# Optimization experiments

Measured on AMD Instinct MI355X. Metric: run time of the kernel, lower is better.

## Reference

```python
import math
import jax, jax.numpy as jnp
import numpy as np

N_HEADS = 16
N_KV_HEADS = 4
HEAD_DIM = 128
D_MODEL = 2048
THETA = 10000.0
SCALE_BASE = 512


def _rope_cos_sin(seq_len, head_dim, theta):
    half = head_dim // 2
    inv_freq = 1.0 / theta ** (jnp.arange(half, dtype=jnp.float32) / half)
    pos = jnp.arange(seq_len, dtype=jnp.float32)
    freqs = jnp.outer(pos, inv_freq)  # (S, half)
    freqs = jnp.concatenate([freqs, freqs], axis=-1)  # (S, D)
    return jnp.cos(freqs), jnp.sin(freqs)


def _rotate_half(x):
    half = x.shape[-1] // 2
    return jnp.concatenate([-x[..., half:], x[..., :half]], axis=-1)


def _xpos_scale(seq_len, head_dim, scale_base):
    pos = jnp.arange(seq_len, dtype=jnp.float32)
    scale = (pos + scale_base / 2.0) / scale_base  # (S,)
    half = head_dim // 2
    s = jnp.broadcast_to(scale[:, None], (seq_len, half))
    # interleave: even idx -> scale, odd idx -> 1/scale
    return jnp.stack([s, 1.0 / s], axis=-1).reshape(seq_len, head_dim)


def setup_inputs() -> dict:
    key = jax.random.key(0)
    ks = jax.random.split(key, 5)
    std = 1.0 / math.sqrt(D_MODEL)
    x = jax.random.normal(ks[0], (2, 2048, D_MODEL), dtype=jnp.float32)
    Wq = jax.random.normal(ks[1], (D_MODEL, N_HEADS * HEAD_DIM), dtype=jnp.float32) * std
    Wk = jax.random.normal(ks[2], (D_MODEL, N_KV_HEADS * HEAD_DIM), dtype=jnp.float32) * std
    Wv = jax.random.normal(ks[3], (D_MODEL, N_KV_HEADS * HEAD_DIM), dtype=jnp.float32) * std
    Wo = jax.random.normal(ks[4], (N_HEADS * HEAD_DIM, D_MODEL), dtype=jnp.float32) * std
    return {"x": x, "Wq": Wq, "Wk": Wk, "Wv": Wv, "Wo": Wo}


def reference(x, Wq, Wk, Wv, Wo):
    B, S, _ = x.shape
    kv_groups = N_HEADS // N_KV_HEADS

    q = (x @ Wq).reshape(B, S, N_HEADS, HEAD_DIM).transpose(0, 2, 1, 3)     # (B,H,S,D)
    k = (x @ Wk).reshape(B, S, N_KV_HEADS, HEAD_DIM).transpose(0, 2, 1, 3)  # (B,Hk,S,D)
    v = (x @ Wv).reshape(B, S, N_KV_HEADS, HEAD_DIM).transpose(0, 2, 1, 3)

    cos, sin = _rope_cos_sin(S, HEAD_DIM, THETA)
    cos = cos[None, None]
    sin = sin[None, None]
    q = q * cos + _rotate_half(q) * sin
    k = k * cos + _rotate_half(k) * sin
    xscale = _xpos_scale(S, HEAD_DIM, SCALE_BASE)[None, None]
    q = q * xscale
    k = k * (1.0 / xscale)

    # GQA: expand kv heads to full head count
    k = jnp.repeat(k, kv_groups, axis=1)  # (B,H,S,D)
    v = jnp.repeat(v, kv_groups, axis=1)

    scale = math.sqrt(HEAD_DIM)
    scores = jnp.einsum('bhqd,bhkd->bhqk', q, k) / scale
    causal = jnp.tril(jnp.ones((S, S), dtype=bool))
    scores = jnp.where(causal[None, None], scores, -jnp.inf)
    attn = jax.nn.softmax(scores, axis=-1)
    out = jnp.einsum('bhqk,bhkd->bhqd', attn, v)
    out = out.transpose(0, 2, 1, 3).reshape(B, S, N_HEADS * HEAD_DIM)
    return out @ Wo
```

## Files before the change

kernel.cpp:

```cpp
#include <hip/hip_runtime.h>
#include <math.h>

#define BDIM 2
#define SLEN 2048
#define NH 16
#define NKV 4
#define HD 128

typedef __attribute__((ext_vector_type(8))) short short8v;
typedef __attribute__((ext_vector_type(4))) short short4v;
typedef __attribute__((ext_vector_type(8))) __bf16 bf16x8;
typedef __attribute__((ext_vector_type(4))) float f32x4;
typedef __attribute__((ext_vector_type(16))) float f32x16;
typedef __attribute__((ext_vector_type(4))) unsigned int u32x4;

__device__ inline unsigned short f2bf(float x) {
  unsigned int u = __builtin_bit_cast(unsigned int, x);
  unsigned int r = (u + 0x7fffu + ((u >> 16) & 1u)) >> 16;
  return (unsigned short)r;
}
__device__ inline float bf2f(unsigned short b) {
  unsigned int u = ((unsigned int)b) << 16;
  return __builtin_bit_cast(float, u);
}
__device__ inline unsigned int pk2(float a, float b) {
  unsigned short ua = __builtin_bit_cast(unsigned short, (__bf16)a);
  unsigned short ub = __builtin_bit_cast(unsigned short, (__bf16)b);
  return (unsigned int)ua | ((unsigned int)ub << 16);
}

template <bool BF16_OUT, bool SPLIT>
__global__ __launch_bounds__(256) void gemm_ring(
    const unsigned short* __restrict__ A, const unsigned short* __restrict__ Bt,
    void* __restrict__ C0, void* __restrict__ C1,
    int M, int N, int K, int Nsplit, int S0, int S1) {
  __shared__ __align__(16) unsigned short lds[3 * 8192];
  const int t    = threadIdx.x;
  const int lane = t & 63;
  const int w    = t >> 6;
  const int lg   = lane >> 4, l15 = lane & 15;
  const int wr   = w >> 1,    wc  = w & 1;
  const int bm = blockIdx.y * 128, bn = blockIdx.x * 128;

  const int r0  = t >> 2;
  const int c8  = (t & 3) ^ (r0 & 3);
  const int dst = t * 8;

#define STAGE(kt, b)                                                           \
  { _Pragma("unroll") for (int i = 0; i < 2; ++i) {                            \
      __builtin_amdgcn_global_load_lds(                                        \
          (const __attribute__((address_space(1))) unsigned int*)              \
              &A[(size_t)(bm + i * 64 + r0) * K + (kt) * 32 + c8 * 8],         \
          (__attribute__((address_space(3))) unsigned int*)                    \
              &lds[(b) * 8192 + i * 2048 + dst],                               \
          16, 0, 0);                                                           \
      __builtin_amdgcn_global_load_lds(                                        \
          (const __attribute__((address_space(1))) unsigned int*)              \
              &Bt[(size_t)(bn + i * 64 + r0) * K + (kt) * 32 + c8 * 8],        \
          (__attribute__((address_space(3))) unsigned int*)                    \
              &lds[(b) * 8192 + 4096 + i * 2048 + dst],                        \
          16, 0, 0);                                                           \
  } }

  f32x4 acc[4][4];
#pragma unroll
  for (int m = 0; m < 4; ++m)
#pragma unroll
    for (int n = 0; n < 4; ++n) acc[m][n] = (f32x4){0.f, 0.f, 0.f, 0.f};

  const int NT = K >> 5;
  STAGE(0, 0)
  STAGE(1, 1)
  int bc = 0;

  for (int kt = 0; kt < NT; ++kt) {
    if (kt + 1 < NT) {
      asm volatile("s_waitcnt vmcnt(4)" ::: "memory");
    } else {
      asm volatile("s_waitcnt vmcnt(0)" ::: "memory");
    }
    __builtin_amdgcn_s_barrier();
    __builtin_amdgcn_sched_barrier(0);

    const unsigned short* As = &lds[bc * 8192];
    const unsigned short* Bs = As + 4096;
    bf16x8 a[4], b[4];
#pragma unroll
    for (int m = 0; m < 4; ++m) {
      const int row = wr * 64 + m * 16 + l15;
      a[m] = __builtin_bit_cast(bf16x8, *reinterpret_cast<const short8v*>(
          &As[row * 32 + ((lg ^ (l15 & 3)) * 8)]));
    }
#pragma unroll
    for (int n = 0; n < 4; ++n) {
      const int row = wc * 64 + n * 16 + l15;
      b[n] = __builtin_bit_cast(bf16x8, *reinterpret_cast<const short8v*>(
          &Bs[row * 32 + ((lg ^ (l15 & 3)) * 8)]));
    }
#pragma unroll
    for (int m = 0; m < 4; ++m)
#pragma unroll
      for (int n = 0; n < 4; ++n)
        acc[m][n] = __builtin_amdgcn_mfma_f32_16x16x32_bf16(a[m], b[n], acc[m][n], 0, 0, 0);

    asm volatile("s_waitcnt lgkmcnt(0)" ::: "memory");
    __builtin_amdgcn_s_barrier();
    __builtin_amdgcn_sched_barrier(0);
    if (kt + 2 < NT) {
      const int nb = bc + 2 >= 3 ? bc - 1 : bc + 2;
      STAGE(kt + 2, nb)
    }
    bc = (bc + 1 >= 3) ? 0 : bc + 1;
  }

  void* dst_p;
  int col0, stride;
  if (!SPLIT || bn < Nsplit) {
    dst_p = C0; col0 = bn; stride = S0;
  } else {
    dst_p = C1; col0 = bn - Nsplit; stride = S1;
  }
#pragma unroll
  for (int m = 0; m < 4; ++m) {
#pragma unroll
    for (int j = 0; j < 4; ++j) {
      const size_t row = (size_t)(bm + wr * 64 + m * 16 + lg * 4 + j);
#pragma unroll
      for (int n = 0; n < 4; ++n) {
        const int col = col0 + wc * 64 + n * 16 + l15;
        if (BF16_OUT)
          ((unsigned short*)dst_p)[row * stride + col] = f2bf(acc[m][n][j]);
        else
          ((float*)dst_p)[row * stride + col] = acc[m][n][j];
      }
    }
  }
#undef STAGE
}

__global__ __launch_bounds__(256) void transpose_cast(
    const float* __restrict__ W, unsigned short* __restrict__ Wt, int K, int N) {
  __shared__ float tile[32][33];
  const int tx = threadIdx.x & 31, ty = threadIdx.x >> 5;
  const int n0 = blockIdx.x * 32, k0 = blockIdx.y * 32;
#pragma unroll
  for (int i = 0; i < 4; ++i)
    tile[ty + i * 8][tx] = W[(size_t)(k0 + ty + i * 8) * N + n0 + tx];
  __syncthreads();
#pragma unroll
  for (int i = 0; i < 4; ++i)
    Wt[(size_t)(n0 + ty + i * 8) * K + k0 + tx] = f2bf(tile[tx][ty + i * 8]);
}

__global__ __launch_bounds__(256) void cast_f32_bf16(
    const float* __restrict__ in, unsigned short* __restrict__ out) {
  const int i = (blockIdx.x * 256 + threadIdx.x) * 8;
  float4 a = *reinterpret_cast<const float4*>(&in[i]);
  float4 b = *reinterpret_cast<const float4*>(&in[i + 4]);
  short8v s;
  s[0] = f2bf(a.x); s[1] = f2bf(a.y); s[2] = f2bf(a.z); s[3] = f2bf(a.w);
  s[4] = f2bf(b.x); s[5] = f2bf(b.y); s[6] = f2bf(b.z); s[7] = f2bf(b.w);
  *reinterpret_cast<short8v*>(&out[i]) = s;
}

__global__ __launch_bounds__(256) void rope_xpos_ip(
    unsigned short* __restrict__ buf, int row_stride, int nh_shift, int invert,
    float extra_scale) {
  const int idx = blockIdx.x * 256 + threadIdx.x;
  const int dp  = idx & 63;
  const int tmp = idx >> 6;
  const int h   = tmp & ((1 << nh_shift) - 1);
  const int row = tmp >> nh_shift;
  const int s   = row & (SLEN - 1);

  const float inv_freq = expf(-(float)dp * (9.210340371976184f / 64.0f));
  const float ang = (float)s * inv_freq;
  float sn, cs;
  sincosf(ang, &sn, &cs);

  unsigned short* p = buf + (size_t)row * row_stride + h * HD;
  const float x0 = bf2f(p[dp]);
  const float x1 = bf2f(p[dp + 64]);
  float y0 = x0 * cs - x1 * sn;
  float y1 = x1 * cs + x0 * sn;

  const float scl = ((float)s + 256.0f) / 512.0f;
  float se_even = invert ? (1.0f / scl) : scl;
  float se_odd  = invert ? scl : (1.0f / scl);
  float se = ((dp & 1) ? se_odd : se_even) * extra_scale;

  p[dp]      = f2bf(y0 * se);
  p[dp + 64] = f2bf(y1 * se);
}

__global__ __launch_bounds__(512) void flash_attn_v10(
    const unsigned short* __restrict__ qb, const unsigned short* __restrict__ kvb,
    unsigned short* __restrict__ o) {
  const int bid = blockIdx.x;
  const int u   = bid & 7;
  const int bh  = bid >> 3;
  const int h   = bh & (NH - 1);
  const int b   = bh >> 4;
  const int kvh = h >> 2;

  __shared__ __align__(16) unsigned char smem[131072];

  const int t    = threadIdx.x;
  const int lane = t & 63;
  const int w    = t >> 6;
  const int par  = w >> 2;
  const int wq   = w & 3;
  const int hi   = lane >> 5;
  const int l31  = lane & 31;

  const size_t bS = (size_t)b * SLEN;

  const int vr2 = t & 31;
  const int vg  = t >> 5;
  int krow[2], kgrp[2];
#pragma unroll
  for (int i = 0; i < 2; ++i) {
    const int slot = w * 2048 + i * 1024 + lane * 16;
    krow[i] = slot >> 8;
    kgrp[i] = (slot >> 4) & 15;
  }

#define K_STAGE(kt, bufk)                                                      \
  { _Pragma("unroll") for (int i = 0; i < 2; ++i) {                            \
      const unsigned short* ksrc = &kvb[(bS + (size_t)(kt) * 64 + krow[i]) * 1024 \
          + kvh * 128 + ((kgrp[i] ^ (krow[i] & 15)) << 3)];                    \
      __builtin_amdgcn_global_load_lds(                                        \
          (const __attribute__((address_space(1))) unsigned int*)ksrc,         \
          (__attribute__((address_space(3))) unsigned int*)                    \
              (smem + (bufk) * 16384 + w * 2048 + i * 1024),                   \
          16, 0, 0); } }

#define V_LOAD(kt, r0, r1)                                                     \
  { const size_t vb_ = (bS + (size_t)(kt) * 64) * 1024 + kvh * 128 + 512;      \
    r0 = *reinterpret_cast<const short8v*>(                                    \
        &kvb[vb_ + (size_t)(2 * vr2) * 1024 + vg * 8]);                        \
    r1 = *reinterpret_cast<const short8v*>(                                    \
        &kvb[vb_ + (size_t)(2 * vr2 + 1) * 1024 + vg * 8]); }

#define V_WRITE(bufk, r0, r1)                                                  \
  { unsigned int* Vw_ = (unsigned int*)(smem + 65536 + (bufk) * 16384);        \
    _Pragma("unroll") for (int j = 0; j < 8; ++j) {                            \
      const int d = vg * 8 + j;                                                \
      Vw_[d * 32 + (vr2 ^ ((d & 7) << 2))] =                                   \
          (unsigned int)(unsigned short)r0[j] |                                \
          ((unsigned int)(unsigned short)r1[j] << 16); } }

  for (int half = 0; half < 2; ++half) {
    const int qt2 = half ? (15 - u) : u;

    bf16x8 qf[8];
    {
      const size_t qrow = (bS + qt2 * 128 + wq * 32 + l31) * 2048 + (size_t)h * HD;
#pragma unroll
      for (int c = 0; c < 8; ++c)
        qf[c] = __builtin_bit_cast(bf16x8,
            *reinterpret_cast<const short8v*>(&qb[qrow + c * 16 + hi * 8]));
    }

    f32x16 Od[4];
#pragma unroll
    for (int ds = 0; ds < 4; ++ds)
#pragma unroll
      for (int r = 0; r < 16; ++r) Od[ds][r] = 0.f;
    float m_run = -1e30f, l_run = 0.f;

    short8v va0, va1, vb0, vb1;

    K_STAGE(0, 0)
    K_STAGE(1, 1)
    V_LOAD(0, va0, va1)
    V_LOAD(1, vb0, vb1)
    V_WRITE(0, va0, va1)
    V_WRITE(1, vb0, vb1)
    __syncthreads();

    for (int e = 0; e <= qt2; ++e) {
      const int s = e & 1;
      const int kt = 2 * e + par;
      const bool more = (e < qt2);
      if (more) {
        K_STAGE(2 * e + 2, (s ^ 1) * 2 + 0)
        K_STAGE(2 * e + 3, (s ^ 1) * 2 + 1)
        V_LOAD(2 * e + 2, va0, va1)
        V_LOAD(2 * e + 3, vb0, vb1)
      }
      const unsigned short* Kb = (const unsigned short*)(smem + (s * 2 + par) * 16384);
      const unsigned int*   Vw = (const unsigned int*)(smem + 65536 + (s * 2 + par) * 16384);

      f32x16 Sa, Sb;
#pragma unroll
      for (int r = 0; r < 16; ++r) { Sa[r] = 0.f; Sb[r] = 0.f; }
      __builtin_amdgcn_s_setprio(1);
#pragma unroll
      for (int c = 0; c < 8; ++c) {
        const int ra = l31, rb = 32 + l31;
        bf16x8 ka = __builtin_bit_cast(bf16x8, *reinterpret_cast<const short8v*>(
            &Kb[ra * 128 + (((2 * c + hi) ^ (ra & 15)) << 3)]));
        bf16x8 kb2 = __builtin_bit_cast(bf16x8, *reinterpret_cast<const short8v*>(
            &Kb[rb * 128 + (((2 * c + hi) ^ (rb & 15)) << 3)]));
        Sa = __builtin_amdgcn_mfma_f32_32x32x16_bf16(ka, qf[c], Sa, 0, 0, 0);
        Sb = __builtin_amdgcn_mfma_f32_32x32x16_bf16(kb2, qf[c], Sb, 0, 0, 0);
      }
      __builtin_amdgcn_s_setprio(0);

      if (kt >= 2 * qt2) {
        const int thresh = qt2 * 128 + wq * 32 + l31 - kt * 64;
#pragma unroll
        for (int r = 0; r < 16; ++r) {
          const int kla = (r & 3) + 8 * (r >> 2) + 4 * hi;
          if (kla > thresh) Sa[r] = -INFINITY;
          if (kla + 32 > thresh) Sb[r] = -INFINITY;
        }
      }

      float pmax = Sa[0];
#pragma unroll
      for (int r = 0; r < 16; ++r) pmax = fmaxf(pmax, fmaxf(Sa[r], Sb[r]));
      pmax = fmaxf(pmax, __shfl_xor(pmax, 32));

      const bool defer = __all(pmax - m_run <= 8.0f);
      float m_new, f;
      if (defer) {
        m_new = m_run; f = 1.0f;
      } else {
        m_new = fmaxf(m_run, pmax);
        f = __expf(m_run - m_new);
        m_run = m_new;
      }

      float psum = 0.f;
#pragma unroll
      for (int r = 0; r < 16; ++r) {
        Sa[r] = __expf(Sa[r] - m_new);
        Sb[r] = __expf(Sb[r] - m_new);
        psum += Sa[r] + Sb[r];
      }
      psum += __shfl_xor(psum, 32);
      l_run = l_run * f + psum;

      if (!defer) {
#pragma unroll
        for (int ds = 0; ds < 4; ++ds)
#pragma unroll
          for (int r = 0; r < 16; ++r) Od[ds][r] *= f;
      }

#pragma unroll
      for (int kc = 0; kc < 4; ++kc) {
        const int Zz = kc & 1;
        f32x16 Sx = (kc >> 1) ? Sb : Sa;
        unsigned int W00 = pk2(Sx[4 * (2 * Zz + 0) + 0], Sx[4 * (2 * Zz + 0) + 1]);
        unsigned int W01 = pk2(Sx[4 * (2 * Zz + 0) + 2], Sx[4 * (2 * Zz + 0) + 3]);
        unsigned int W10 = pk2(Sx[4 * (2 * Zz + 1) + 0], Sx[4 * (2 * Zz + 1) + 1]);
        unsigned int W11 = pk2(Sx[4 * (2 * Zz + 1) + 2], Sx[4 * (2 * Zz + 1) + 3]);
        unsigned int X00 = __shfl_xor(W00, 32), X01 = __shfl_xor(W01, 32);
        unsigned int X10 = __shfl_xor(W10, 32), X11 = __shfl_xor(W11, 32);
        u32x4 pv;
        pv[0] = hi ? X10 : W00;
        pv[1] = hi ? X11 : W01;
        pv[2] = hi ? W10 : X00;
        pv[3] = hi ? W11 : X01;
        bf16x8 pf = __builtin_bit_cast(bf16x8, pv);
        __builtin_amdgcn_s_setprio(1);
#pragma unroll
        for (int ds = 0; ds < 4; ++ds) {
          const int d = ds * 32 + l31;
          u32x4 vv = *reinterpret_cast<const u32x4*>(
              &Vw[d * 32 + ((kc * 8 + hi * 4) ^ ((d & 7) << 2))]);
          bf16x8 vf = __builtin_bit_cast(bf16x8, vv);
          Od[ds] = __builtin_amdgcn_mfma_f32_32x32x16_bf16(vf, pf, Od[ds], 0, 0, 0);
        }
        __builtin_amdgcn_s_setprio(0);
      }

      if (more) {
        V_WRITE((s ^ 1) * 2 + 0, va0, va1)
        V_WRITE((s ^ 1) * 2 + 1, vb0, vb1)
      }
      __syncthreads();
    }

    float* mf = (float*)smem;
    float* Of = (float*)(smem + 2048);
    if (par == 1) {
      mf[(wq * 2 + 0) * 64 + lane] = m_run;
      mf[(wq * 2 + 1) * 64 + lane] = l_run;
    }
    float fe = 0.f, fo = 0.f, linv = 0.f;
#pragma unroll
    for (int p = 0; p < 2; ++p) {
      if (par == 1) {
#pragma unroll
        for (int d2 = 0; d2 < 2; ++d2)
#pragma unroll
          for (int r = 0; r < 16; ++r)
            Of[((wq * 2 + d2) * 16 + r) * 64 + lane] = Od[p * 2 + d2][r];
      }
      __syncthreads();
      if (par == 0) {
        if (p == 0) {
          const float m_o = mf[(wq * 2 + 0) * 64 + lane];
          const float l_o = mf[(wq * 2 + 1) * 64 + lane];
          const float mm = fmaxf(m_run, m_o);
          fe = __expf(m_run - mm);
          fo = __expf(m_o - mm);
          linv = 1.0f / (l_run * fe + l_o * fo);
        }
        const size_t row = bS + qt2 * 128 + wq * 32 + l31;
#pragma unroll
        for (int d2 = 0; d2 < 2; ++d2) {
          const int ds = p * 2 + d2;
#pragma unroll
          for (int g = 0; g < 4; ++g) {
            short4v ov;
#pragma unroll
            for (int j = 0; j < 4; ++j) {
              const int r = g * 4 + j;
              const float val = (Od[ds][r] * fe +
                                 Of[((wq * 2 + d2) * 16 + r) * 64 + lane] * fo) * linv;
              ov[j] = (short)__builtin_bit_cast(unsigned short, (__bf16)val);
            }
            const int dbase = ds * 32 + 8 * g + 4 * hi;
            *reinterpret_cast<short4v*>(&o[row * 2048 + h * HD + dbase]) = ov;
          }
        }
      }
      __syncthreads();
    }
  }
#undef K_STAGE
#undef V_LOAD
#undef V_WRITE
}

extern "C" void kernel_launch(void* const* d_in, const int* in_sizes, int n_in,
                              void* d_out, int out_size, void* d_ws, size_t ws_size,
                              hipStream_t stream) {
  (void)in_sizes; (void)n_in; (void)out_size; (void)ws_size;
  const float* x  = (const float*)d_in[0];
  const float* Wq = (const float*)d_in[1];
  const float* Wk = (const float*)d_in[2];
  const float* Wv = (const float*)d_in[3];
  const float* Wo = (const float*)d_in[4];
  float* out = (float*)d_out;

  unsigned char* ws = (unsigned char*)d_ws;
  const size_t MB = 1024 * 1024;
  unsigned short* xb    = (unsigned short*)(ws);
  unsigned short* Wqkvt = (unsigned short*)(ws + 16 * MB);
  unsigned short* Wot   = (unsigned short*)(ws + 28 * MB);
  unsigned short* qb    = (unsigned short*)(ws + 36 * MB);
  unsigned short* kvb   = (unsigned short*)(ws + 52 * MB);
  unsigned short* attn  = (unsigned short*)(ws + 60 * MB);

  const int M = BDIM * SLEN;
  dim3 blk(256);

  cast_f32_bf16<<<(M * 2048) / (256 * 8), blk, 0, stream>>>(x, xb);
  transpose_cast<<<dim3(64, 64), blk, 0, stream>>>(Wq, Wqkvt, 2048, 2048);
  transpose_cast<<<dim3(16, 64), blk, 0, stream>>>(
      Wk, Wqkvt + (size_t)2048 * 2048, 2048, 512);
  transpose_cast<<<dim3(16, 64), blk, 0, stream>>>(
      Wv, Wqkvt + (size_t)2560 * 2048, 2048, 512);
  transpose_cast<<<dim3(64, 64), blk, 0, stream>>>(Wo, Wot, 2048, 2048);

  gemm_ring<true, true><<<dim3(24, 32), blk, 0, stream>>>(
      xb, Wqkvt, qb, kvb, M, 3072, 2048, 2048, 2048, 1024);

  rope_xpos_ip<<<(M * NH * 64) / 256, blk, 0, stream>>>(
      qb, 2048, 4, 0, 0.088388347648318447f);
  rope_xpos_ip<<<(M * NKV * 64) / 256, blk, 0, stream>>>(kvb, 1024, 2, 1, 1.0f);

  flash_attn_v10<<<BDIM * NH * 8, dim3(512), 0, stream>>>(qb, kvb, attn);

  gemm_ring<false, false><<<dim3(16, 32), blk, 0, stream>>>(
      attn, Wot, out, nullptr, M, 2048, 2048, 2048, 2048, 0);
}
```

Measured before the change: 220.0 us.

## Pre-transpose V and fuse Q RoPE/xPos into attention Q load

Adds a separate kernel that transposes V into a d-major layout so the attention kernel can stage V with asynchronous global-to-LDS loads, like K, instead of register loads followed by scattered LDS writes. The Q RoPE/xPos pass is removed and applied in registers when the attention kernel loads its Q fragments. This drops one full read-modify-write pass over Q and a register staging step in the inner loop. In exchange it adds a transpose launch, extra workspace traffic, and transcendental math per Q load in the attention kernel.

```diff
diff --git a/kernel.cpp b/kernel.cpp
--- a/kernel.cpp
+++ b/kernel.cpp
@@ -193,9 +193,42 @@
   p[dp + 64] = f2bf(y1 * se);
 }
 
-__global__ __launch_bounds__(512) void flash_attn_v10(
+__global__ __launch_bounds__(256) void transpose_v(
+    const unsigned short* __restrict__ kvb, unsigned short* __restrict__ vt) {
+  const int bid = blockIdx.x;
+  const int st  = bid & 31;
+  const int kvh = (bid >> 5) & 3;
+  const int b   = bid >> 7;
+  __shared__ unsigned short tile[64][136];
+  const int t = threadIdx.x;
+
+#pragma unroll
+  for (int i = 0; i < 4; ++i) {
+    const int idx = t + i * 256;
+    const int s   = idx >> 4;
+    const int d0  = (idx & 15) * 8;
+    short8v v = *reinterpret_cast<const short8v*>(
+        &kvb[((size_t)(b * SLEN + st * 64 + s)) * 1024 + 512 + kvh * 128 + d0]);
+    *reinterpret_cast<short8v*>(&tile[s][d0]) = v;
+  }
+  __syncthreads();
+#pragma unroll
+  for (int i = 0; i < 4; ++i) {
+    const int idx = t + i * 256;
+    const int d   = idx >> 3;
+    const int cc  = idx & 7;
+    const int cs  = cc ^ (d & 7);
+    short8v o;
+#pragma unroll
+    for (int j = 0; j < 8; ++j) o[j] = (short)tile[cs * 8 + j][d];
+    *reinterpret_cast<short8v*>(
+        &vt[(((size_t)(b * 4 + kvh) * 128 + d) * 2048) + st * 64 + cc * 8]) = o;
+  }
+}
+
+__global__ __launch_bounds__(512) void flash_attn_v11(
     const unsigned short* __restrict__ qb, const unsigned short* __restrict__ kvb,
-    unsigned short* __restrict__ o) {
+    const unsigned short* __restrict__ vt, unsigned short* __restrict__ o) {
   const int bid = blockIdx.x;
   const int u   = bid & 7;
   const int bh  = bid >> 3;
@@ -214,15 +247,21 @@
   const int l31  = lane & 31;
 
   const size_t bS = (size_t)b * SLEN;
-
-  const int vr2 = t & 31;
-  const int vg  = t >> 5;
+  const size_t vbase = (size_t)(b * 4 + kvh) * 128;
+
   int krow[2], kgrp[2];
 #pragma unroll
   for (int i = 0; i < 2; ++i) {
     const int slot = w * 2048 + i * 1024 + lane * 16;
     krow[i] = slot >> 8;
     kgrp[i] = (slot >> 4) & 15;
+  }
+  int vrow[2], vchk[2];
+#pragma unroll
+  for (int i = 0; i < 2; ++i) {
+    const int slot = w * 2048 + i * 1024 + lane * 16;
+    vrow[i] = slot >> 7;
+    vchk[i] = (slot >> 4) & 7;
   }
 
 #define K_STAGE(kt, bufk)                                                      \
@@ -235,31 +274,48 @@
               (smem + (bufk) * 16384 + w * 2048 + i * 1024),                   \
           16, 0, 0); } }
 
-#define V_LOAD(kt, r0, r1)                                                     \
-  { const size_t vb_ = (bS + (size_t)(kt) * 64) * 1024 + kvh * 128 + 512;      \
-    r0 = *reinterpret_cast<const short8v*>(                                    \
-        &kvb[vb_ + (size_t)(2 * vr2) * 1024 + vg * 8]);                        \
-    r1 = *reinterpret_cast<const short8v*>(                                    \
-        &kvb[vb_ + (size_t)(2 * vr2 + 1) * 1024 + vg * 8]); }
-
-#define V_WRITE(bufk, r0, r1)                                                  \
-  { unsigned int* Vw_ = (unsigned int*)(smem + 65536 + (bufk) * 16384);        \
-    _Pragma("unroll") for (int j = 0; j < 8; ++j) {                            \
-      const int d = vg * 8 + j;                                                \
-      Vw_[d * 32 + (vr2 ^ ((d & 7) << 2))] =                                   \
-          (unsigned int)(unsigned short)r0[j] |                                \
-          ((unsigned int)(unsigned short)r1[j] << 16); } }
+#define V_STAGE(kt, bufk)                                                      \
+  { _Pragma("unroll") for (int i = 0; i < 2; ++i) {                            \
+      const unsigned short* vsrc = &vt[(vbase + vrow[i]) * 2048                \
+          + (size_t)(kt) * 64 + vchk[i] * 8];                                  \
+      __builtin_amdgcn_global_load_lds(                                        \
+          (const __attribute__((address_space(1))) unsigned int*)vsrc,         \
+          (__attribute__((address_space(3))) unsigned int*)                    \
+              (smem + 65536 + (bufk) * 16384 + w * 2048 + i * 1024),           \
+          16, 0, 0); } }
 
   for (int half = 0; half < 2; ++half) {
     const int qt2 = half ? (15 - u) : u;
 
     bf16x8 qf[8];
     {
-      const size_t qrow = (bS + qt2 * 128 + wq * 32 + l31) * 2048 + (size_t)h * HD;
+      const int spos = qt2 * 128 + wq * 32 + l31;
+      const size_t qrow = (bS + spos) * 2048 + (size_t)h * HD;
+      short8v qr[8];
 #pragma unroll
       for (int c = 0; c < 8; ++c)
-        qf[c] = __builtin_bit_cast(bf16x8,
-            *reinterpret_cast<const short8v*>(&qb[qrow + c * 16 + hi * 8]));
+        qr[c] = *reinterpret_cast<const short8v*>(&qb[qrow + c * 16 + hi * 8]);
+      const float scl = ((float)spos + 256.0f) / 512.0f;
+      const float se_e = scl * 0.088388347648318447f;
+      const float se_o = (1.0f / scl) * 0.088388347648318447f;
+#pragma unroll
+      for (int c = 0; c < 4; ++c) {
+        short8v nlo, nhi;
+#pragma unroll
+        for (int j = 0; j < 8; ++j) {
+          const int dp = c * 16 + hi * 8 + j;
+          const float inv_freq = expf(-(float)dp * (9.210340371976184f / 64.0f));
+          float sn, cs;
+          sincosf((float)spos * inv_freq, &sn, &cs);
+          const float x0 = bf2f((unsigned short)qr[c][j]);
+          const float x1 = bf2f((unsigned short)qr[c + 4][j]);
+          const float se = (j & 1) ? se_o : se_e;
+          nlo[j] = (short)f2bf((x0 * cs - x1 * sn) * se);
+          nhi[j] = (short)f2bf((x1 * cs + x0 * sn) * se);
+        }
+        qf[c]     = __builtin_bit_cast(bf16x8, nlo);
+        qf[c + 4] = __builtin_bit_cast(bf16x8, nhi);
+      }
     }
 
     f32x16 Od[4];
@@ -269,14 +325,10 @@
       for (int r = 0; r < 16; ++r) Od[ds][r] = 0.f;
     float m_run = -1e30f, l_run = 0.f;
 
-    short8v va0, va1, vb0, vb1;
-
     K_STAGE(0, 0)
     K_STAGE(1, 1)
-    V_LOAD(0, va0, va1)
-    V_LOAD(1, vb0, vb1)
-    V_WRITE(0, va0, va1)
-    V_WRITE(1, vb0, vb1)
+    V_STAGE(0, 0)
+    V_STAGE(1, 1)
     __syncthreads();
 
     for (int e = 0; e <= qt2; ++e) {
@@ -286,8 +338,8 @@
       if (more) {
         K_STAGE(2 * e + 2, (s ^ 1) * 2 + 0)
         K_STAGE(2 * e + 3, (s ^ 1) * 2 + 1)
-        V_LOAD(2 * e + 2, va0, va1)
-        V_LOAD(2 * e + 3, vb0, vb1)
+        V_STAGE(2 * e + 2, (s ^ 1) * 2 + 0)
+        V_STAGE(2 * e + 3, (s ^ 1) * 2 + 1)
       }
       const unsigned short* Kb = (const unsigned short*)(smem + (s * 2 + par) * 16384);
       const unsigned int*   Vw = (const unsigned int*)(smem + 65536 + (s * 2 + par) * 16384);
@@ -378,10 +430,6 @@
         __builtin_amdgcn_s_setprio(0);
       }
 
-      if (more) {
-        V_WRITE((s ^ 1) * 2 + 0, va0, va1)
-        V_WRITE((s ^ 1) * 2 + 1, vb0, vb1)
-      }
       __syncthreads();
     }
 
@@ -434,8 +482,7 @@
     }
   }
 #undef K_STAGE
-#undef V_LOAD
-#undef V_WRITE
+#undef V_STAGE
 }
 
 extern "C" void kernel_launch(void* const* d_in, const int* in_sizes, int n_in,
@@ -457,6 +504,7 @@
   unsigned short* qb    = (unsigned short*)(ws + 36 * MB);
   unsigned short* kvb   = (unsigned short*)(ws + 52 * MB);
   unsigned short* attn  = (unsigned short*)(ws + 60 * MB);
+  unsigned short* vtb   = (unsigned short*)(ws + 76 * MB);
 
   const int M = BDIM * SLEN;
   dim3 blk(256);
@@ -472,11 +520,10 @@
   gemm_ring<true, true><<<dim3(24, 32), blk, 0, stream>>>(
       xb, Wqkvt, qb, kvb, M, 3072, 2048, 2048, 2048, 1024);
 
-  rope_xpos_ip<<<(M * NH * 64) / 256, blk, 0, stream>>>(
-      qb, 2048, 4, 0, 0.088388347648318447f);
   rope_xpos_ip<<<(M * NKV * 64) / 256, blk, 0, stream>>>(kvb, 1024, 2, 1, 1.0f);
-
-  flash_attn_v10<<<BDIM * NH * 8, dim3(512), 0, stream>>>(qb, kvb, attn);
+  transpose_v<<<256, blk, 0, stream>>>(kvb, vtb);
+
+  flash_attn_v11<<<BDIM * NH * 8, dim3(512), 0, stream>>>(qb, kvb, vtb, attn);
 
   gemm_ring<false, false><<<dim3(16, 32), blk, 0, stream>>>(
       attn, Wot, out, nullptr, M, 2048, 2048, 2048, 2048, 0);
```

New measurement: 215.1 us. -2.2%, faster.
